# Performance work log

Hardware: AMD Instinct MI355X
Metric: run time of the kernel (lower is better)

## Reference

```python
import jax, jax.numpy as jnp
import numpy as np

B, U = 64, 512            # batch, max_units
AE = 1024
UE = 256                  # unit_embedding_size
A = 256                   # target_head_attention_size


def setup_inputs() -> dict:
    key = jax.random.key(0)
    ks = jax.random.split(key, 10)
    return {
        "autoregressive_embedding": jax.random.normal(ks[0], (B, U, AE), jnp.float32),
        "own_unit_embeddings": jax.random.normal(ks[1], (B, U, UE), jnp.float32),
        "enemy_unit_embeddings": jax.random.normal(ks[2], (B, U, UE), jnp.float32),
        "nr_own_units": jax.random.randint(ks[3], (B, 1), 0, U).astype(jnp.int64),
        "nr_units_enemy": jax.random.randint(ks[4], (B, 1), 0, U).astype(jnp.int64),
        "nr_own_flags": jax.random.randint(ks[5], (B, 1), 0, 8).astype(jnp.int64),
        "Wq": jax.random.normal(ks[6], (UE + AE, A), jnp.float32) * (1.0 / np.sqrt(UE + AE)),
        "bq": jnp.zeros((A,), jnp.float32),
        "Wk": jax.random.normal(ks[7], (UE, A), jnp.float32) * (1.0 / np.sqrt(UE)),
        "bk": jnp.zeros((A,), jnp.float32),
    }


def reference(autoregressive_embedding, own_unit_embeddings, enemy_unit_embeddings,
              nr_own_units, nr_units_enemy, nr_own_flags, Wq, bq, Wk, bk):
    # combined: [B, U, AE+UE]
    combined = jnp.concatenate([autoregressive_embedding, own_unit_embeddings], axis=2)
    queries = combined @ Wq + bq                       # [B, U, A]
    keys = enemy_unit_embeddings @ Wk + bk             # [B, U, A]
    attention = jnp.einsum("bqd,bkd->bqk", queries, keys) / (A ** 0.5)  # [B, U, U]
    # Vectorized mask: rows in [nr_own_flags, nr_own_units), cols in [0, nr_units_enemy)
    idx = jnp.arange(U)
    row_ok = (idx[None, :] >= nr_own_flags) & (idx[None, :] < nr_own_units)  # [B, U]
    col_ok = idx[None, :] < nr_units_enemy                                   # [B, U]
    mask = jnp.where(row_ok[:, :, None] & col_ok[:, None, :], 1.0, 1e-9)     # [B, U, U]
    return jax.nn.softmax(attention * mask, axis=-1)
```

## Files before the change

### kernel.cpp

```cpp
#include <hip/hip_runtime.h>

constexpr int B  = 64;
constexpr int U  = 512;
constexpr int AE = 1024;
constexpr int UE = 256;
constexpr int A  = 256;
constexpr int KQ = AE + UE;

typedef _Float16 f16x8 __attribute__((ext_vector_type(8)));
typedef float    f32x4 __attribute__((ext_vector_type(4)));

__global__ void prep(const float* __restrict__ Wq, const float* __restrict__ Wk,
                     _Float16* __restrict__ WqT, _Float16* __restrict__ WkT) {
    int idx = blockIdx.x * 256 + threadIdx.x;
    if (idx < KQ * A) {
        int k = idx >> 8, n = idx & 255;
        WqT[(size_t)n * KQ + k] = (_Float16)Wq[idx];
    } else {
        int j = idx - KQ * A;
        if (j < A * A) {
            int k = j >> 8, n = j & 255;
            WkT[(size_t)n * A + k] = (_Float16)Wk[j];
        }
    }
}

__global__ __launch_bounds__(512) void gemm(
    const float* __restrict__ A1, int s1, int split,
    const float* __restrict__ A2, int s2,
    const _Float16* __restrict__ BT,
    const float* __restrict__ bias,
    _Float16* __restrict__ Out,
    int Ktot)
{
    __shared__ __align__(16) _Float16 Al[2][64][32];
    __shared__ __align__(16) _Float16 Bl[2][256][32];

    const int t    = threadIdx.x;
    const int lane = t & 63;
    const int w    = t >> 6;
    const int mbase = blockIdx.x * 64;

    const int wm = (w & 1) * 32;
    const int wn = (w >> 1) * 64;

    f32x4 acc[2][4] = {};

    const int ar  = t >> 3;
    const int aq  = t & 7;
    const int ap  = aq >> 2;
    const int asw = ((aq & 3) ^ ((ar >> 1) & 3)) * 8;
    const size_t grow = mbase + ar;

    int bp[4], bn[4], bq[4], bsw[4];
    #pragma unroll
    for (int j = 0; j < 4; j++) {
        int s = j * 512 + t;
        bp[j] = s >> 10;
        bn[j] = (s & 1023) >> 2;
        bq[j] = s & 3;
        bsw[j] = ((bq[j] ^ ((bn[j] >> 1) & 3))) * 8;
    }

    float4 areg0, areg1;
    f16x8 breg[4];

    auto loadA = [&](int k0) {
        int kg = k0 + aq * 8;
        const float* src = (kg < split) ? (A1 + grow * (size_t)s1 + kg)
                                        : (A2 + grow * (size_t)s2 + (kg - split));
        areg0 = ((const float4*)src)[0];
        areg1 = ((const float4*)src)[1];
    };
    auto loadB = [&](int k0) {
        #pragma unroll
        for (int j = 0; j < 4; j++)
            breg[j] = *(const f16x8*)(BT + (size_t)bn[j] * Ktot + k0 + bp[j] * 32 + bq[j] * 8);
    };

    loadA(0);
    loadB(0);

    const int rsw = (((lane & 15) >> 1) & 3);
    const int nk = Ktot >> 6;
    for (int kb = 0; kb < nk; kb++) {
        __syncthreads();
        {
            f16x8 hv;
            hv[0] = (_Float16)areg0.x; hv[1] = (_Float16)areg0.y;
            hv[2] = (_Float16)areg0.z; hv[3] = (_Float16)areg0.w;
            hv[4] = (_Float16)areg1.x; hv[5] = (_Float16)areg1.y;
            hv[6] = (_Float16)areg1.z; hv[7] = (_Float16)areg1.w;
            *(f16x8*)(&Al[ap][ar][asw]) = hv;
            #pragma unroll
            for (int j = 0; j < 4; j++)
                *(f16x8*)(&Bl[bp[j]][bn[j]][bsw[j]]) = breg[j];
        }
        __syncthreads();
        if (kb + 1 < nk) { loadA(kb * 64 + 64); loadB(kb * 64 + 64); }
        #pragma unroll
        for (int p = 0; p < 2; p++) {
            f16x8 af[2], bf[4];
            #pragma unroll
            for (int mt = 0; mt < 2; mt++)
                af[mt] = *(const f16x8*)(&Al[p][wm + mt * 16 + (lane & 15)][(((lane >> 4) ^ rsw)) * 8]);
            #pragma unroll
            for (int nt = 0; nt < 4; nt++)
                bf[nt] = *(const f16x8*)(&Bl[p][wn + nt * 16 + (lane & 15)][(((lane >> 4) ^ rsw)) * 8]);
            #pragma unroll
            for (int mt = 0; mt < 2; mt++)
                #pragma unroll
                for (int nt = 0; nt < 4; nt++)
                    acc[mt][nt] = __builtin_amdgcn_mfma_f32_16x16x32_f16(
                        af[mt], bf[nt], acc[mt][nt], 0, 0, 0);
        }
    }
    const int col0 = wn + (lane & 15);
    const int rsub = (lane >> 4) * 4;
    #pragma unroll
    for (int nt = 0; nt < 4; nt++) {
        const int col = col0 + nt * 16;
        const float bv = bias[col];
        const int c5 = col >> 5, c31 = col & 31;
        #pragma unroll
        for (int mt = 0; mt < 2; mt++)
            #pragma unroll
            for (int r = 0; r < 4; r++) {
                int row = mbase + wm + mt * 16 + rsub + r;
                int bb = row >> 9, u = row & 511;
                Out[(((size_t)bb * 8 + c5) * 512 + u) * 32 + c31] =
                    (_Float16)(acc[mt][nt][r] + bv);
            }
    }
}

__global__ __launch_bounds__(512) void attn(
    const _Float16* __restrict__ Qh, const _Float16* __restrict__ Kh,
    const int* __restrict__ nr_own_units, const int* __restrict__ nr_units_enemy,
    const int* __restrict__ nr_own_flags, float* __restrict__ Out)
{
    __shared__ __align__(16) _Float16 Ql[8][64][32];
    __shared__ __align__(16) _Float16 Kl[512][32];
    __shared__ float red[64][4];

    const int t    = threadIdx.x;
    const int lane = t & 63;
    const int w    = t >> 6;
    const int b    = blockIdx.y;
    const int qbase = blockIdx.x * 64;

    const int nf = nr_own_flags[b];
    const int nu = nr_own_units[b];
    const int ne = nr_units_enemy[b];

    const int wm = (w & 1) * 32;
    const int wn = (w >> 1) * 128;

    f16x8 qreg[4];
    {
        const _Float16* Qb = Qh + ((size_t)b * 8 * 512 + qbase) * 32;
        #pragma unroll
        for (int j = 0; j < 4; j++) {
            int s = j * 512 + t;
            int p = s >> 8, row = (s & 255) >> 2, cq = s & 3;
            qreg[j] = *(const f16x8*)(Qb + ((size_t)p * 512 + row) * 32 + cq * 8);
        }
        #pragma unroll
        for (int j = 0; j < 4; j++) {
            int s = j * 512 + t;
            int p = s >> 8, row = (s & 255) >> 2, cq = s & 3;
            *(f16x8*)(&Ql[p][row][(cq ^ ((row >> 1) & 3)) * 8]) = qreg[j];
        }
    }

    const _Float16* Kb = Kh + (size_t)b * 8 * 512 * 32;
    f16x8 kreg[4];
    const int krow = t >> 2;
    const int kq   = t & 3;
    auto loadK = [&](int c) {
        const _Float16* Kc = Kb + (size_t)c * 512 * 32;
        #pragma unroll
        for (int j = 0; j < 4; j++)
            kreg[j] = *(const f16x8*)(Kc + ((size_t)(j * 128 + krow)) * 32 + kq * 8);
    };
    loadK(0);

    f32x4 acc[2][8] = {};
    const int rsw = (((lane & 15) >> 1) & 3);
    for (int c = 0; c < 8; c++) {
        __syncthreads();
        #pragma unroll
        for (int j = 0; j < 4; j++) {
            int row = j * 128 + krow;
            *(f16x8*)(&Kl[row][(kq ^ ((row >> 1) & 3)) * 8]) = kreg[j];
        }
        __syncthreads();
        if (c < 7) loadK(c + 1);
        f16x8 af[2], bf[8];
        #pragma unroll
        for (int mt = 0; mt < 2; mt++)
            af[mt] = *(const f16x8*)(&Ql[c][wm + mt * 16 + (lane & 15)][((lane >> 4) ^ rsw) * 8]);
        #pragma unroll
        for (int nt = 0; nt < 8; nt++)
            bf[nt] = *(const f16x8*)(&Kl[wn + nt * 16 + (lane & 15)][((lane >> 4) ^ rsw) * 8]);
        #pragma unroll
        for (int mt = 0; mt < 2; mt++)
            #pragma unroll
            for (int nt = 0; nt < 8; nt++)
                acc[mt][nt] = __builtin_amdgcn_mfma_f32_16x16x32_f16(
                    af[mt], bf[nt], acc[mt][nt], 0, 0, 0);
    }

    const int rsub = (lane >> 4) * 4;
    #pragma unroll
    for (int mt = 0; mt < 2; mt++)
        #pragma unroll
        for (int nt = 0; nt < 8; nt++)
            #pragma unroll
            for (int r = 0; r < 4; r++) {
                int rl = wm + mt * 16 + rsub + r;
                int uq = qbase + rl;
                int col = wn + nt * 16 + (lane & 15);
                bool ok = (col < ne) && (uq >= nf) && (uq < nu);
                acc[mt][nt][r] = acc[mt][nt][r] * 0.0625f * (ok ? 1.0f : 1e-9f);
            }

    float mx[2][4];
    #pragma unroll
    for (int mt = 0; mt < 2; mt++)
        #pragma unroll
        for (int r = 0; r < 4; r++) {
            float m = acc[mt][0][r];
            #pragma unroll
            for (int nt = 1; nt < 8; nt++) m = fmaxf(m, acc[mt][nt][r]);
            #pragma unroll
            for (int off = 1; off <= 8; off <<= 1) m = fmaxf(m, __shfl_xor(m, off));
            mx[mt][r] = m;
        }
    if ((lane & 15) == 0) {
        #pragma unroll
        for (int mt = 0; mt < 2; mt++)
            #pragma unroll
            for (int r = 0; r < 4; r++)
                red[wm + mt * 16 + rsub + r][w >> 1] = mx[mt][r];
    }
    __syncthreads();
    #pragma unroll
    for (int mt = 0; mt < 2; mt++)
        #pragma unroll
        for (int r = 0; r < 4; r++) {
            f32x4 v = *(const f32x4*)(&red[wm + mt * 16 + rsub + r][0]);
            mx[mt][r] = fmaxf(fmaxf(v[0], v[1]), fmaxf(v[2], v[3]));
        }
    __syncthreads();

    float sm[2][4];
    #pragma unroll
    for (int mt = 0; mt < 2; mt++)
        #pragma unroll
        for (int r = 0; r < 4; r++) {
            float s = 0.f;
            #pragma unroll
            for (int nt = 0; nt < 8; nt++) {
                float e = __expf(acc[mt][nt][r] - mx[mt][r]);
                acc[mt][nt][r] = e;
                s += e;
            }
            #pragma unroll
            for (int off = 1; off <= 8; off <<= 1) s += __shfl_xor(s, off);
            sm[mt][r] = s;
        }
    if ((lane & 15) == 0) {
        #pragma unroll
        for (int mt = 0; mt < 2; mt++)
            #pragma unroll
            for (int r = 0; r < 4; r++)
                red[wm + mt * 16 + rsub + r][w >> 1] = sm[mt][r];
    }
    __syncthreads();

    #pragma unroll
    for (int mt = 0; mt < 2; mt++)
        #pragma unroll
        for (int r = 0; r < 4; r++) {
            int rl = wm + mt * 16 + rsub + r;
            f32x4 v = *(const f32x4*)(&red[rl][0]);
            float inv = 1.0f / (v[0] + v[1] + v[2] + v[3]);
            float* orow = Out + ((size_t)b * 512 + qbase + rl) * 512 + wn + (lane & 15);
            #pragma unroll
            for (int nt = 0; nt < 8; nt++)
                orow[nt * 16] = acc[mt][nt][r] * inv;
        }
}

extern "C" void kernel_launch(void* const* d_in, const int* in_sizes, int n_in,
                              void* d_out, int out_size, void* d_ws, size_t ws_size,
                              hipStream_t stream) {
    const float* ar    = (const float*)d_in[0];
    const float* own   = (const float*)d_in[1];
    const float* enemy = (const float*)d_in[2];
    const int*   n_own   = (const int*)d_in[3];
    const int*   n_enemy = (const int*)d_in[4];
    const int*   n_flags = (const int*)d_in[5];
    const float* Wq = (const float*)d_in[6];
    const float* bq = (const float*)d_in[7];
    const float* Wk = (const float*)d_in[8];
    const float* bk = (const float*)d_in[9];
    float* out = (float*)d_out;

    char* ws = (char*)d_ws;
    _Float16* WqT = (_Float16*)(ws);
    _Float16* WkT = (_Float16*)(ws + 655360);
    _Float16* Qh  = (_Float16*)(ws + 786432);
    _Float16* Kh  = (_Float16*)(ws + 786432 + 16777216);

    prep<<<dim3((KQ * A + A * A) / 256), dim3(256), 0, stream>>>(Wq, Wk, WqT, WkT);

    gemm<<<dim3(512), dim3(512), 0, stream>>>(ar, AE, AE, own, UE, WqT, bq, Qh, KQ);
    gemm<<<dim3(512), dim3(512), 0, stream>>>(enemy, UE, 0, enemy, UE, WkT, bk, Kh, A);

    attn<<<dim3(8, B), dim3(512), 0, stream>>>(Qh, Kh, n_own, n_enemy, n_flags, out);
}
```

Baseline: 330.6 us.

## Halve GEMM M-tile to 32 rows and double grid for occupancy

The projection GEMM now uses a 32-row M tile per block instead of 64, with each of the 8 waves owning a 32-column N slice, and the grid doubles to 1024 blocks. The shared-memory A and B load mappings and swizzles are reworked to match, and launch bounds request 8 waves per EU. The aim is more parallelism and occupancy across the CUs for this memory-bound fp32-input GEMM. The cost is that the fp16 weight tile is reloaded twice as often, and each wave now reuses its B fragments across fewer rows.

```diff
diff --git a/kernel.cpp b/kernel.cpp
--- a/kernel.cpp
+++ b/kernel.cpp
@@ -8,6 +8,7 @@
 constexpr int KQ = AE + UE;
 
 typedef _Float16 f16x8 __attribute__((ext_vector_type(8)));
+typedef _Float16 f16x4 __attribute__((ext_vector_type(4)));
 typedef float    f32x4 __attribute__((ext_vector_type(4)));
 
 __global__ void prep(const float* __restrict__ Wq, const float* __restrict__ Wk,
@@ -25,7 +26,7 @@
     }
 }
 
-__global__ __launch_bounds__(512) void gemm(
+__global__ __launch_bounds__(512, 8) void gemm(
     const float* __restrict__ A1, int s1, int split,
     const float* __restrict__ A2, int s2,
     const _Float16* __restrict__ BT,
@@ -33,84 +34,76 @@
     _Float16* __restrict__ Out,
     int Ktot)
 {
-    __shared__ __align__(16) _Float16 Al[2][64][32];
+    __shared__ __align__(16) _Float16 Al[2][32][32];
     __shared__ __align__(16) _Float16 Bl[2][256][32];
 
     const int t    = threadIdx.x;
     const int lane = t & 63;
     const int w    = t >> 6;
-    const int mbase = blockIdx.x * 64;
-
-    const int wm = (w & 1) * 32;
-    const int wn = (w >> 1) * 64;
-
-    f32x4 acc[2][4] = {};
-
-    const int ar  = t >> 3;
-    const int aq  = t & 7;
-    const int ap  = aq >> 2;
-    const int asw = ((aq & 3) ^ ((ar >> 1) & 3)) * 8;
+    const int mbase = blockIdx.x * 32;
+
+    const int wn = w * 32;
+
+    f32x4 acc[2][2] = {};
+
+    const int ar  = t >> 4;
+    const int aq  = t & 15;
+    const int ap  = aq >> 3;
+    const int ah  = (aq & 7) * 4;
+    const int asw = ((ah >> 3) ^ ((ar >> 1) & 3)) * 8 + (ah & 7);
     const size_t grow = mbase + ar;
 
-    int bp[4], bn[4], bq[4], bsw[4];
-    #pragma unroll
-    for (int j = 0; j < 4; j++) {
-        int s = j * 512 + t;
-        bp[j] = s >> 10;
-        bn[j] = (s & 1023) >> 2;
-        bq[j] = s & 3;
-        bsw[j] = ((bq[j] ^ ((bn[j] >> 1) & 3))) * 8;
-    }
-
-    float4 areg0, areg1;
+    const int brow = t >> 1;
+    const int bpl  = t & 1;
+    const int bsw  = (brow >> 1) & 3;
+
+    float4 areg;
     f16x8 breg[4];
 
     auto loadA = [&](int k0) {
-        int kg = k0 + aq * 8;
+        int kg = k0 + aq * 4;
         const float* src = (kg < split) ? (A1 + grow * (size_t)s1 + kg)
                                         : (A2 + grow * (size_t)s2 + (kg - split));
-        areg0 = ((const float4*)src)[0];
-        areg1 = ((const float4*)src)[1];
+        areg = *(const float4*)src;
     };
     auto loadB = [&](int k0) {
+        const _Float16* src = BT + (size_t)brow * Ktot + k0 + bpl * 32;
         #pragma unroll
         for (int j = 0; j < 4; j++)
-            breg[j] = *(const f16x8*)(BT + (size_t)bn[j] * Ktot + k0 + bp[j] * 32 + bq[j] * 8);
+            breg[j] = *(const f16x8*)(src + j * 8);
     };
 
     loadA(0);
     loadB(0);
 
-    const int rsw = (((lane & 15) >> 1) & 3);
+    const int rp = ((lane >> 4) ^ ((lane >> 1) & 3)) * 8;
     const int nk = Ktot >> 6;
     for (int kb = 0; kb < nk; kb++) {
         __syncthreads();
         {
-            f16x8 hv;
-            hv[0] = (_Float16)areg0.x; hv[1] = (_Float16)areg0.y;
-            hv[2] = (_Float16)areg0.z; hv[3] = (_Float16)areg0.w;
-            hv[4] = (_Float16)areg1.x; hv[5] = (_Float16)areg1.y;
-            hv[6] = (_Float16)areg1.z; hv[7] = (_Float16)areg1.w;
-            *(f16x8*)(&Al[ap][ar][asw]) = hv;
+            f16x4 hv;
+            hv[0] = (_Float16)areg.x; hv[1] = (_Float16)areg.y;
+            hv[2] = (_Float16)areg.z; hv[3] = (_Float16)areg.w;
+            *(f16x4*)(&Al[ap][ar][asw]) = hv;
             #pragma unroll
             for (int j = 0; j < 4; j++)
-                *(f16x8*)(&Bl[bp[j]][bn[j]][bsw[j]]) = breg[j];
+                *(f16x8*)(&Bl[bpl][brow][(j ^ bsw) * 8]) = breg[j];
         }
         __syncthreads();
         if (kb + 1 < nk) { loadA(kb * 64 + 64); loadB(kb * 64 + 64); }
         #pragma unroll
         for (int p = 0; p < 2; p++) {
-            f16x8 af[2], bf[4];
+            f16x8 af[2], bf[2];
             #pragma unroll
             for (int mt = 0; mt < 2; mt++)
-                af[mt] = *(const f16x8*)(&Al[p][wm + mt * 16 + (lane & 15)][(((lane >> 4) ^ rsw)) * 8]);
-            #pragma unroll
-            for (int nt = 0; nt < 4; nt++)
-                bf[nt] = *(const f16x8*)(&Bl[p][wn + nt * 16 + (lane & 15)][(((lane >> 4) ^ rsw)) * 8]);
+                af[mt] = *(const f16x8*)(&Al[p][mt * 16 + (lane & 15)][rp]);
+            #pragma unroll
+            for (int nt = 0; nt < 2; nt++)
+                bf[nt] = *(const f16x8*)(&Bl[p][wn + nt * 16 + (lane & 15)][rp]);
             #pragma unroll
             for (int mt = 0; mt < 2; mt++)
                 #pragma unroll
-                for (int nt = 0; nt < 4; nt++)
+                for (int nt = 0; nt < 2; nt++)
                     acc[mt][nt] = __builtin_amdgcn_mfma_f32_16x16x32_f16(
                         af[mt], bf[nt], acc[mt][nt], 0, 0, 0);
         }
@@ -118,7 +111,7 @@
     const int col0 = wn + (lane & 15);
     const int rsub = (lane >> 4) * 4;
     #pragma unroll
-    for (int nt = 0; nt < 4; nt++) {
+    for (int nt = 0; nt < 2; nt++) {
         const int col = col0 + nt * 16;
         const float bv = bias[col];
         const int c5 = col >> 5, c31 = col & 31;
@@ -126,7 +119,7 @@
         for (int mt = 0; mt < 2; mt++)
             #pragma unroll
             for (int r = 0; r < 4; r++) {
-                int row = mbase + wm + mt * 16 + rsub + r;
+                int row = mbase + mt * 16 + rsub + r;
                 int bb = row >> 9, u = row & 511;
                 Out[(((size_t)bb * 8 + c5) * 512 + u) * 32 + c31] =
                     (_Float16)(acc[mt][nt][r] + bv);
@@ -316,8 +309,8 @@
 
     prep<<<dim3((KQ * A + A * A) / 256), dim3(256), 0, stream>>>(Wq, Wk, WqT, WkT);
 
-    gemm<<<dim3(512), dim3(512), 0, stream>>>(ar, AE, AE, own, UE, WqT, bq, Qh, KQ);
-    gemm<<<dim3(512), dim3(512), 0, stream>>>(enemy, UE, 0, enemy, UE, WkT, bk, Kh, A);
+    gemm<<<dim3(1024), dim3(512), 0, stream>>>(ar, AE, AE, own, UE, WqT, bq, Qh, KQ);
+    gemm<<<dim3(1024), dim3(512), 0, stream>>>(enemy, UE, 0, enemy, UE, WkT, bk, Kh, A);
 
     attn<<<dim3(8, B), dim3(512), 0, stream>>>(Qh, Kh, n_own, n_enemy, n_flags, out);
 }
```

Measured after the change: 367.1 us. 11.0% more time.
